# Performance work log

Hardware: AMD Instinct MI355X
Metric: run time of the kernel (lower is better)

## Reference

```python
import jax, jax.numpy as jnp
import numpy as np

B, CIN, COUT, G, HEADS = 4, 256, 256, 8, 4
K, S, P = 7, 1, 3
H = W = 32
IN_W = CIN // G
OUT_W = COUT // G


def setup_inputs() -> dict:
    key = jax.random.key(0)
    ks = jax.random.split(key, 9)
    def n(k, shape, scale=1.0):
        return jax.random.normal(k, shape, dtype=jnp.float32) * scale
    # kaiming fan_out init for the 1x1 convs (fan_out = out channels)
    return {
        "x": n(ks[0], (B, CIN, H, W)),
        "wq": n(ks[1], (G, OUT_W * HEADS, IN_W), (2.0 / (OUT_W * HEADS)) ** 0.5),
        "bq": n(ks[2], (G, OUT_W * HEADS), 0.01),
        "wk": n(ks[3], (G, OUT_W, IN_W), (2.0 / OUT_W) ** 0.5),
        "bk": n(ks[4], (G, OUT_W), 0.01),
        "wv": n(ks[5], (G, OUT_W, IN_W), (2.0 / OUT_W) ** 0.5),
        "bv": n(ks[6], (G, OUT_W), 0.01),
        "rel_h": n(ks[7], (OUT_W // 2, 1, 1, G, K, 1)),
        "rel_w": n(ks[8], (OUT_W // 2, 1, 1, G, 1, K)),
    }


def _sparse_conv(x, w, b):
    # grouped 1x1 conv, groups stacked on last axis (matches torch.stack(dim=-1))
    # x: [B, G*I, h, w]; w: [G, O, I]; b: [G, O] -> [B, O, h, w, G]
    Bn, C, hh, ww = x.shape
    xr = x.reshape(Bn, G, C // G, hh, ww)
    out = jnp.einsum('bgihw,goi->bohwg', xr, w)
    return out + b.T[None, :, None, None, :]


def _unfold(x5, k, s):
    # x5: [B, C, Hp, Wp, G] -> [B, C, Ho, Wo, G, k, k]  (torch unfold(2).unfold(3))
    Bn, C, Hp, Wp, Gn = x5.shape
    Ho = (Hp - k) // s + 1
    Wo = (Wp - k) // s + 1
    patches = jnp.stack(
        [x5[:, :, i:i + (Ho - 1) * s + 1:s, j:j + (Wo - 1) * s + 1:s, :]
         for i in range(k) for j in range(k)], axis=-1)
    return patches.reshape(Bn, C, Ho, Wo, Gn, k, k)


def reference(x, wq, bq, wk, bk, wv, bv, rel_h, rel_w):
    xp = jnp.pad(x, ((0, 0), (0, 0), (P, P), (P, P)))
    q = _sparse_conv(x, wq, bq)    # [B, OUT_W*HEADS, H, W, G]
    k = _sparse_conv(xp, wk, bk)   # [B, OUT_W, Hp, Wp, G] (bias at padded locations, as in torch)
    v = _sparse_conv(xp, wv, bv)
    k = _unfold(k, K, S)           # [B, OUT_W, H, W, G, K, K]
    v = _unfold(v, K, S)
    kh, kw = jnp.split(k, 2, axis=1)
    k = jnp.concatenate([kh + rel_h, kw + rel_w], axis=1)
    kf = k.reshape(B, OUT_W, H, W, G * K * K)
    vf = v.reshape(B, OUT_W, H, W, G * K * K)
    q = q.reshape(B, HEADS, OUT_W, H, W, G)
    # scores: sum over channel c; softmax over flattened (group, kh, kw) window
    scores = jnp.einsum('bhcxyg,bcxym->bhxygm', q, kf)
    attn = jax.nn.softmax(scores, axis=-1)
    # weighted sum over window m and heads h (matches sum(dim=1) then sum(dim=-1))
    out = jnp.einsum('bhxygm,bcxym->bcxyg', attn, vf)   # [B, OUT_W, H, W, G]
    out = jnp.transpose(out, (0, 4, 2, 3, 1)).reshape(B, -1, H, W)  # transpose(1,-1)+reshape
    return out
```

## Files before the change

### kernel.cpp

```cpp
#include <hip/hip_runtime.h>
#include <math.h>

typedef _Float16 f16;
typedef _Float16 f16x4 __attribute__((ext_vector_type(4)));
typedef _Float16 f16x8 __attribute__((ext_vector_type(8)));
typedef __bf16 bf16x4 __attribute__((ext_vector_type(4)));
typedef __bf16 bf16x4a8 __attribute__((ext_vector_type(4), aligned(8)));
typedef short s16x4 __attribute__((ext_vector_type(4)));
typedef float f32x4 __attribute__((ext_vector_type(4)));
typedef unsigned int u32;

#define MFMA_F16(a, b, c)  __builtin_amdgcn_mfma_f32_16x16x32_f16(a, b, c, 0, 0, 0)
#define MFMA_BF16_K16(a, b, c) __builtin_amdgcn_mfma_f32_16x16x16bf16_1k(a, b, c, 0, 0, 0)

static __device__ inline f16x8 cvt8(const float* p) {
    const float4* p4 = (const float4*)p;
    float4 u0 = p4[0], u1 = p4[1];
    f16x8 r;
    r[0] = (f16)u0.x; r[1] = (f16)u0.y; r[2] = (f16)u0.z; r[3] = (f16)u0.w;
    r[4] = (f16)u1.x; r[5] = (f16)u1.y; r[6] = (f16)u1.z; r[7] = (f16)u1.w;
    return r;
}

static __device__ inline u32 alignsel(u32 hi, u32 lo, u32 sh) {
    return sh ? (u32)(((((unsigned long long)hi) << 32) | lo) >> sh) : lo;
}

static __device__ inline u32 pack2bf(float a, float b) {
    __bf16 x0 = (__bf16)a, x1 = (__bf16)b;
    return (u32)__builtin_bit_cast(unsigned short, x0) |
           ((u32)__builtin_bit_cast(unsigned short, x1) << 16);
}

__global__ __launch_bounds__(256) void produce_kernel(
    const float* __restrict__ x,
    const float* __restrict__ wq, const float* __restrict__ bq,
    const float* __restrict__ wk, const float* __restrict__ bk,
    const float* __restrict__ wv, const float* __restrict__ bv,
    const float* __restrict__ rel_h, const float* __restrict__ rel_w,
    f16* __restrict__ Qb, f16* __restrict__ Kb,
    __bf16* __restrict__ Vb, f16* __restrict__ relp) {
    int bid = blockIdx.x;
    int t = threadIdx.x;

    if (bid == 1216) {
        for (int idx = t; idx < 2944; idx += 256) {
            float v;
            if (idx < 896) {
                int c = idx & 15, gk = idx >> 4;
                v = rel_h[c * 56 + gk];
            } else {
                int i2 = idx - 896;
                int c = i2 & 31, gw = i2 >> 5;
                int g = gw >> 3, kw = gw & 7;
                v = (c >= 16 && kw < 7) ? rel_w[(c - 16) * 56 + g * 7 + kw] : 0.f;
            }
            relp[idx] = (f16)v;
        }
        return;
    }

    int hp = bid % 38, g = (bid / 38) & 7, b = bid / 304;
    bool hin = (hp >= 3 && hp < 35);
    size_t kvbase = (size_t)(b * 8 + g);
    u32* Vb32 = (u32*)Vb;

    if (!hin) {
        for (int idx = t; idx < 38 * 32; idx += 256) {
            int wp = idx >> 5, c = idx & 31;
            Kb[((kvbase * 38 + hp) * 38 + wp) * 32 + c] = (f16)bk[g * 32 + c];
        }
        for (int idx = t; idx < 704; idx += 256) {
            int c = idx / 22, dw = idx - c * 22;
            float bb = bv[g * 32 + c];
            float v0 = (dw * 2 <= 37) ? bb : 0.f;
            float v1 = (dw * 2 + 1 <= 37) ? bb : 0.f;
            Vb32[((kvbase * 38 + hp) * 32 + c) * 22 + dw] = pack2bf(v0, v1);
        }
        return;
    }

    int h = hp - 3;
    __shared__ __align__(16) f16 xTl[32 * 40];
    __shared__ float vt[32 * 44];

    {
        int ic = t >> 3, w = (t & 7) * 4;
        float4 xv = *(const float4*)(x + (((size_t)b * 256 + g * 32 + ic) * 32 + h) * 32 + w);
        xTl[(w + 0) * 40 + ic] = (f16)xv.x;
        xTl[(w + 1) * 40 + ic] = (f16)xv.y;
        xTl[(w + 2) * 40 + ic] = (f16)xv.z;
        xTl[(w + 3) * 40 + ic] = (f16)xv.w;
    }
    for (int idx = t; idx < 384; idx += 256) {
        int c = idx & 31, wi = idx >> 5;
        float bb = bv[g * 32 + c];
        if (wi < 3) vt[c * 44 + wi] = bb;
        else if (wi < 6) vt[c * 44 + 32 + wi] = bb;
        else vt[c * 44 + 32 + wi] = 0.f;
    }
    __syncthreads();

    int l15 = t & 15, quad = (t >> 4) & 3, wave = t >> 6;

    f16x8 xf0 = *(const f16x8*)(xTl + l15 * 40 + quad * 8);
    f16x8 xf1 = *(const f16x8*)(xTl + (16 + l15) * 40 + quad * 8);

#pragma unroll
    for (int i = 0; i < 2; ++i) {
        int mq = wave * 2 + i;
        f16x8 wf = cvt8(wq + ((size_t)g * 128 + mq * 16 + l15) * 32 + quad * 8);
        float4 b4 = *(const float4*)(bq + g * 128 + mq * 16 + quad * 4);
#pragma unroll
        for (int Nt = 0; Nt < 2; ++Nt) {
            f32x4 d = {0.f, 0.f, 0.f, 0.f};
            d = MFMA_F16(wf, Nt ? xf1 : xf0, d);
            f16x4 q4;
            q4[0] = (f16)(d[0] + b4.x); q4[1] = (f16)(d[1] + b4.y);
            q4[2] = (f16)(d[2] + b4.z); q4[3] = (f16)(d[3] + b4.w);
            int w = Nt * 16 + l15;
            *(f16x4*)(Qb + (size_t)((b * 32 + h) * 32 + w) * 1024 + g * 128 + mq * 16 + quad * 4) = q4;
        }
    }

    if (wave < 2) {
        f16x8 wf = cvt8(wk + ((size_t)g * 32 + wave * 16 + l15) * 32 + quad * 8);
        float4 b4 = *(const float4*)(bk + g * 32 + wave * 16 + quad * 4);
#pragma unroll
        for (int Nt = 0; Nt < 2; ++Nt) {
            f32x4 d = {0.f, 0.f, 0.f, 0.f};
            d = MFMA_F16(wf, Nt ? xf1 : xf0, d);
            f16x4 k4;
            k4[0] = (f16)(d[0] + b4.x); k4[1] = (f16)(d[1] + b4.y);
            k4[2] = (f16)(d[2] + b4.z); k4[3] = (f16)(d[3] + b4.w);
            int wp = Nt * 16 + l15 + 3;
            *(f16x4*)(Kb + ((kvbase * 38 + hp) * 38 + wp) * 32 + wave * 16 + quad * 4) = k4;
        }
    } else {
        int Nt = wave - 2;
        f16x8 wf = cvt8(wv + ((size_t)g * 32 + Nt * 16 + l15) * 32 + quad * 8);
        float bias = bv[g * 32 + Nt * 16 + l15];
        int c = Nt * 16 + l15;
#pragma unroll
        for (int Mt = 0; Mt < 2; ++Mt) {
            f32x4 d = {0.f, 0.f, 0.f, 0.f};
            d = MFMA_F16(Mt ? xf1 : xf0, wf, d);
            int wp0 = Mt * 16 + quad * 4 + 3;
            vt[c * 44 + wp0 + 0] = d[0] + bias;
            vt[c * 44 + wp0 + 1] = d[1] + bias;
            vt[c * 44 + wp0 + 2] = d[2] + bias;
            vt[c * 44 + wp0 + 3] = d[3] + bias;
        }
    }

    for (int idx = t; idx < 192; idx += 256) {
        int wi = idx >> 5, c = idx & 31;
        int wp = (wi < 3) ? wi : (32 + wi);
        Kb[((kvbase * 38 + hp) * 38 + wp) * 32 + c] = (f16)bk[g * 32 + c];
    }
    __syncthreads();

    for (int idx = t; idx < 704; idx += 256) {
        int c = idx / 22, dw = idx - c * 22;
        Vb32[((kvbase * 38 + hp) * 32 + c) * 22 + dw] =
            pack2bf(vt[c * 44 + dw * 2], vt[c * 44 + dw * 2 + 1]);
    }
}

__global__ __launch_bounds__(512, 1) void attn_kernel(
    const f16* __restrict__ Qb, const f16* __restrict__ Kb,
    const __bf16* __restrict__ Vb, const f16* __restrict__ relp,
    float* __restrict__ out) {
    __shared__ __align__(16) f16 Klds[33600];
    __shared__ __align__(16) __bf16 Vlds[35840];
    __shared__ __align__(16) f16 Trw_l[2048];

    int bid = blockIdx.x;
    int t = threadIdx.x;
    int G = (bid & 7) * 64 + (bid >> 3);
    int yq = G & 3, x = (G >> 2) & 31, b = G >> 7;
    int y0 = yq * 8;
    int b8 = b * 8;

    int wvi = t >> 6;
    int lane = t & 63;
    int l15 = lane & 15, quad = lane >> 4, kwl = lane & 7, p8 = (lane >> 3) & 1;
    bool oddq = (quad & 1);
    int y = y0 + wvi;
    int pid = (b * 32 + x) * 32 + y;

    f16x8 qf[2];
    {
        const f16* qp = Qb + (size_t)pid * 1024;
        qf[0] = *(const f16x8*)(qp + l15 * 32 + quad * 8);
        qf[1] = *(const f16x8*)(qp + (16 + l15) * 32 + quad * 8);
    }

    for (int i = t; i < 3360; i += 512) {
        int row = i >> 2, q = i & 3;
        int g = row / 105, r2 = row - g * 105;
        int kh = r2 / 15, wpl = r2 - kh * 15;
        int wp = y0 + wpl; if (wp > 37) wp = 37;
        f16x8 kv = *(const f16x8*)(Kb + (((size_t)(b8 + g) * 38 + x + kh) * 38 + wp) * 32 + q * 8);
        if (q < 2) kv += *(const f16x8*)(relp + (g * 7 + kh) * 16 + q * 8);
        *(f16x8*)(Klds + row * 40 + q * 8) = kv;
    }
    for (int i = t; i < 8960; i += 512) {
        int row = i / 5, j = i - row * 5;
        int g = row / 224, r2 = row - g * 224;
        int kh = r2 >> 5, c = r2 & 31;
        uint2 v = *(const uint2*)(Vb + (((size_t)(b8 + g) * 38 + x + kh) * 32 + c) * 44 + y0 + j * 4);
        *(uint2*)(Vlds + row * 20 + j * 4) = v;
    }
    {
        int i = t;
        *(uint2*)(Trw_l + i * 4) = *(const uint2*)(relp + 896 + i * 4);
    }
    __syncthreads();

    float fsumT[2] = {0.f, 0.f};
    f32x4 acc[2][2];
#pragma unroll
    for (int ct = 0; ct < 2; ++ct)
#pragma unroll
        for (int m = 0; m < 2; ++m) acc[ct][m] = (f32x4){0.f, 0.f, 0.f, 0.f};

    int wpl37 = 37 - y0;
    int wplk = wvi + kwl; if (wplk > wpl37) wplk = wpl37;
    u32 shsel = (wvi & 1) ? 16u : 0u;
    bool hi4 = (wvi & 2) != 0;
    int eA = ((quad & 1) + (wvi >> 2)) * 4;

#pragma unroll
    for (int chunk = 0; chunk < 4; ++chunk) {
        int gpr = chunk * 2 + p8;
        int gpv = chunk * 2 + (quad >> 1);
        f16x8 rp = *(const f16x8*)(Trw_l + (gpr * 8 + kwl) * 32 + quad * 8);
        const f16* kp = Klds + (gpr * 105 + wplk) * 40 + quad * 8;
        const __bf16* vb0 = Vlds + (size_t)gpv * 4480 + l15 * 20 + eA;
        const __bf16* vb1 = vb0 + 320;
#pragma unroll
        for (int kh = 0; kh < 7; ++kh) {
            f16x8 kb = *(const f16x8*)kp;  kp += 600;
            kb += rp;
            uint2 A0 = *(const uint2*)vb0;
            uint2 B0 = *(const uint2*)(vb0 + 4);
            uint2 A1 = *(const uint2*)vb1;
            uint2 B1 = *(const uint2*)(vb1 + 4);
            vb0 += 640; vb1 += 640;
            u32 a0 = hi4 ? A0.y : A0.x, a1 = hi4 ? B0.x : A0.y, a2 = hi4 ? B0.y : B0.x;
            s16x4 vf0 = __builtin_bit_cast(s16x4,
                make_uint2(alignsel(a1, a0, shsel), alignsel(a2, a1, shsel)));
            u32 c0 = hi4 ? A1.y : A1.x, c1 = hi4 ? B1.x : A1.y, c2 = hi4 ? B1.y : B1.x;
            s16x4 vf1 = __builtin_bit_cast(s16x4,
                make_uint2(alignsel(c1, c0, shsel), alignsel(c2, c1, shsel)));
#pragma unroll
            for (int Mt = 0; Mt < 2; ++Mt) {
                f32x4 d = {0.f, 0.f, 0.f, 0.f};
                d = MFMA_F16(kb, qf[Mt], d);
                float e0 = __expf(d[0]);
                float e1 = __expf(d[1]);
                float e2 = __expf(d[2]);
                float e3 = oddq ? 0.f : __expf(d[3]);
                fsumT[Mt] += (e0 + e1) + (e2 + e3);
                bf16x4 pb;
                pb[0] = (__bf16)e0; pb[1] = (__bf16)e1;
                pb[2] = (__bf16)e2; pb[3] = (__bf16)e3;
                s16x4 pbi = __builtin_bit_cast(s16x4, pb);
                acc[0][Mt] = MFMA_BF16_K16(vf0, pbi, acc[0][Mt]);
                acc[1][Mt] = MFMA_BF16_K16(vf1, pbi, acc[1][Mt]);
            }
        }
    }

#pragma unroll
    for (int m = 0; m < 2; ++m) {
        fsumT[m] += __shfl_xor(fsumT[m], 16);
        fsumT[m] += __shfl_xor(fsumT[m], 32);
    }
    float inv[2] = {1.0f / fsumT[0], 1.0f / fsumT[1]};

#pragma unroll
    for (int Mt = 0; Mt < 2; ++Mt)
#pragma unroll
        for (int ct = 0; ct < 2; ++ct) {
            float v[4];
#pragma unroll
            for (int r = 0; r < 4; ++r) {
                v[r] = acc[ct][Mt][r] * inv[Mt];
                v[r] += __shfl_xor(v[r], 1);
                v[r] += __shfl_xor(v[r], 2);
            }
            if ((l15 & 3) == 0) {
                int g = Mt * 4 + (l15 >> 2);
                float4 o4 = {v[0], v[1], v[2], v[3]};
                *(float4*)(out + ((((size_t)(b8 + g) * 32 + x) * 32 + y) << 5) +
                           ct * 16 + quad * 4) = o4;
            }
        }
}

extern "C" void kernel_launch(void* const* d_in, const int* in_sizes, int n_in,
                              void* d_out, int out_size, void* d_ws, size_t ws_size,
                              hipStream_t stream) {
    const float* x     = (const float*)d_in[0];
    const float* wq    = (const float*)d_in[1];
    const float* bq    = (const float*)d_in[2];
    const float* wk    = (const float*)d_in[3];
    const float* bk    = (const float*)d_in[4];
    const float* wv    = (const float*)d_in[5];
    const float* bv    = (const float*)d_in[6];
    const float* rel_h = (const float*)d_in[7];
    const float* rel_w = (const float*)d_in[8];
    float* out = (float*)d_out;

    unsigned char* ws = (unsigned char*)d_ws;
    f16*    Qb   = (f16*)ws;
    f16*    Kb   = (f16*)(ws + 8388608);
    __bf16* Vb   = (__bf16*)(ws + 8388608 + 2957312);
    f16*    relp = (f16*)(ws + 8388608 + 2957312 + 3424256);

    hipLaunchKernelGGL(produce_kernel, dim3(1217), dim3(256), 0, stream,
                       x, wq, bq, wk, bk, wv, bv, rel_h, rel_w, Qb, Kb, Vb, relp);
    hipLaunchKernelGGL(attn_kernel, dim3(512), dim3(512), 0, stream,
                       Qb, Kb, Vb, relp, out);
}
```

Before: 121.6 us.

## Fuse QKV projection into attention kernel, computing K/V tiles in LDS

Removes the separate produce kernel and its global Q/K/V workspace. Each attention block now loads its 7-row x halo directly from the fp32 input and runs the 1x1 grouped convs with MFMA, writing K (with rel_h folded in), V and Q straight into LDS. This drops one launch and the global round trip of intermediates. In exchange, neighbouring blocks recompute overlapping K/V halo rows, and the x loads are scalar strided reads.

```diff
diff --git a/kernel.cpp b/kernel.cpp
--- a/kernel.cpp
+++ b/kernel.cpp
@@ -5,7 +5,6 @@
 typedef _Float16 f16x4 __attribute__((ext_vector_type(4)));
 typedef _Float16 f16x8 __attribute__((ext_vector_type(8)));
 typedef __bf16 bf16x4 __attribute__((ext_vector_type(4)));
-typedef __bf16 bf16x4a8 __attribute__((ext_vector_type(4), aligned(8)));
 typedef short s16x4 __attribute__((ext_vector_type(4)));
 typedef float f32x4 __attribute__((ext_vector_type(4)));
 typedef unsigned int u32;
@@ -26,159 +25,22 @@
     return sh ? (u32)(((((unsigned long long)hi) << 32) | lo) >> sh) : lo;
 }
 
-static __device__ inline u32 pack2bf(float a, float b) {
-    __bf16 x0 = (__bf16)a, x1 = (__bf16)b;
-    return (u32)__builtin_bit_cast(unsigned short, x0) |
-           ((u32)__builtin_bit_cast(unsigned short, x1) << 16);
-}
-
-__global__ __launch_bounds__(256) void produce_kernel(
+__global__ __launch_bounds__(512, 1) void fused_kernel(
     const float* __restrict__ x,
     const float* __restrict__ wq, const float* __restrict__ bq,
     const float* __restrict__ wk, const float* __restrict__ bk,
     const float* __restrict__ wv, const float* __restrict__ bv,
     const float* __restrict__ rel_h, const float* __restrict__ rel_w,
-    f16* __restrict__ Qb, f16* __restrict__ Kb,
-    __bf16* __restrict__ Vb, f16* __restrict__ relp) {
-    int bid = blockIdx.x;
-    int t = threadIdx.x;
-
-    if (bid == 1216) {
-        for (int idx = t; idx < 2944; idx += 256) {
-            float v;
-            if (idx < 896) {
-                int c = idx & 15, gk = idx >> 4;
-                v = rel_h[c * 56 + gk];
-            } else {
-                int i2 = idx - 896;
-                int c = i2 & 31, gw = i2 >> 5;
-                int g = gw >> 3, kw = gw & 7;
-                v = (c >= 16 && kw < 7) ? rel_w[(c - 16) * 56 + g * 7 + kw] : 0.f;
-            }
-            relp[idx] = (f16)v;
-        }
-        return;
-    }
-
-    int hp = bid % 38, g = (bid / 38) & 7, b = bid / 304;
-    bool hin = (hp >= 3 && hp < 35);
-    size_t kvbase = (size_t)(b * 8 + g);
-    u32* Vb32 = (u32*)Vb;
-
-    if (!hin) {
-        for (int idx = t; idx < 38 * 32; idx += 256) {
-            int wp = idx >> 5, c = idx & 31;
-            Kb[((kvbase * 38 + hp) * 38 + wp) * 32 + c] = (f16)bk[g * 32 + c];
-        }
-        for (int idx = t; idx < 704; idx += 256) {
-            int c = idx / 22, dw = idx - c * 22;
-            float bb = bv[g * 32 + c];
-            float v0 = (dw * 2 <= 37) ? bb : 0.f;
-            float v1 = (dw * 2 + 1 <= 37) ? bb : 0.f;
-            Vb32[((kvbase * 38 + hp) * 32 + c) * 22 + dw] = pack2bf(v0, v1);
-        }
-        return;
-    }
-
-    int h = hp - 3;
-    __shared__ __align__(16) f16 xTl[32 * 40];
-    __shared__ float vt[32 * 44];
-
-    {
-        int ic = t >> 3, w = (t & 7) * 4;
-        float4 xv = *(const float4*)(x + (((size_t)b * 256 + g * 32 + ic) * 32 + h) * 32 + w);
-        xTl[(w + 0) * 40 + ic] = (f16)xv.x;
-        xTl[(w + 1) * 40 + ic] = (f16)xv.y;
-        xTl[(w + 2) * 40 + ic] = (f16)xv.z;
-        xTl[(w + 3) * 40 + ic] = (f16)xv.w;
-    }
-    for (int idx = t; idx < 384; idx += 256) {
-        int c = idx & 31, wi = idx >> 5;
-        float bb = bv[g * 32 + c];
-        if (wi < 3) vt[c * 44 + wi] = bb;
-        else if (wi < 6) vt[c * 44 + 32 + wi] = bb;
-        else vt[c * 44 + 32 + wi] = 0.f;
-    }
-    __syncthreads();
-
-    int l15 = t & 15, quad = (t >> 4) & 3, wave = t >> 6;
-
-    f16x8 xf0 = *(const f16x8*)(xTl + l15 * 40 + quad * 8);
-    f16x8 xf1 = *(const f16x8*)(xTl + (16 + l15) * 40 + quad * 8);
-
-#pragma unroll
-    for (int i = 0; i < 2; ++i) {
-        int mq = wave * 2 + i;
-        f16x8 wf = cvt8(wq + ((size_t)g * 128 + mq * 16 + l15) * 32 + quad * 8);
-        float4 b4 = *(const float4*)(bq + g * 128 + mq * 16 + quad * 4);
-#pragma unroll
-        for (int Nt = 0; Nt < 2; ++Nt) {
-            f32x4 d = {0.f, 0.f, 0.f, 0.f};
-            d = MFMA_F16(wf, Nt ? xf1 : xf0, d);
-            f16x4 q4;
-            q4[0] = (f16)(d[0] + b4.x); q4[1] = (f16)(d[1] + b4.y);
-            q4[2] = (f16)(d[2] + b4.z); q4[3] = (f16)(d[3] + b4.w);
-            int w = Nt * 16 + l15;
-            *(f16x4*)(Qb + (size_t)((b * 32 + h) * 32 + w) * 1024 + g * 128 + mq * 16 + quad * 4) = q4;
-        }
-    }
-
-    if (wave < 2) {
-        f16x8 wf = cvt8(wk + ((size_t)g * 32 + wave * 16 + l15) * 32 + quad * 8);
-        float4 b4 = *(const float4*)(bk + g * 32 + wave * 16 + quad * 4);
-#pragma unroll
-        for (int Nt = 0; Nt < 2; ++Nt) {
-            f32x4 d = {0.f, 0.f, 0.f, 0.f};
-            d = MFMA_F16(wf, Nt ? xf1 : xf0, d);
-            f16x4 k4;
-            k4[0] = (f16)(d[0] + b4.x); k4[1] = (f16)(d[1] + b4.y);
-            k4[2] = (f16)(d[2] + b4.z); k4[3] = (f16)(d[3] + b4.w);
-            int wp = Nt * 16 + l15 + 3;
-            *(f16x4*)(Kb + ((kvbase * 38 + hp) * 38 + wp) * 32 + wave * 16 + quad * 4) = k4;
-        }
-    } else {
-        int Nt = wave - 2;
-        f16x8 wf = cvt8(wv + ((size_t)g * 32 + Nt * 16 + l15) * 32 + quad * 8);
-        float bias = bv[g * 32 + Nt * 16 + l15];
-        int c = Nt * 16 + l15;
-#pragma unroll
-        for (int Mt = 0; Mt < 2; ++Mt) {
-            f32x4 d = {0.f, 0.f, 0.f, 0.f};
-            d = MFMA_F16(Mt ? xf1 : xf0, wf, d);
-            int wp0 = Mt * 16 + quad * 4 + 3;
-            vt[c * 44 + wp0 + 0] = d[0] + bias;
-            vt[c * 44 + wp0 + 1] = d[1] + bias;
-            vt[c * 44 + wp0 + 2] = d[2] + bias;
-            vt[c * 44 + wp0 + 3] = d[3] + bias;
-        }
-    }
-
-    for (int idx = t; idx < 192; idx += 256) {
-        int wi = idx >> 5, c = idx & 31;
-        int wp = (wi < 3) ? wi : (32 + wi);
-        Kb[((kvbase * 38 + hp) * 38 + wp) * 32 + c] = (f16)bk[g * 32 + c];
-    }
-    __syncthreads();
-
-    for (int idx = t; idx < 704; idx += 256) {
-        int c = idx / 22, dw = idx - c * 22;
-        Vb32[((kvbase * 38 + hp) * 32 + c) * 22 + dw] =
-            pack2bf(vt[c * 44 + dw * 2], vt[c * 44 + dw * 2 + 1]);
-    }
-}
-
-__global__ __launch_bounds__(512, 1) void attn_kernel(
-    const f16* __restrict__ Qb, const f16* __restrict__ Kb,
-    const __bf16* __restrict__ Vb, const f16* __restrict__ relp,
     float* __restrict__ out) {
     __shared__ __align__(16) f16 Klds[33600];
     __shared__ __align__(16) __bf16 Vlds[35840];
-    __shared__ __align__(16) f16 Trw_l[2048];
+    __shared__ __align__(16) f16 Qlds[8192];
+    __shared__ __align__(16) f16 TrwL[2048];
 
     int bid = blockIdx.x;
     int t = threadIdx.x;
     int G = (bid & 7) * 64 + (bid >> 3);
-    int yq = G & 3, x = (G >> 2) & 31, b = G >> 7;
+    int yq = G & 3, xx = (G >> 2) & 31, b = G >> 7;
     int y0 = yq * 8;
     int b8 = b * 8;
 
@@ -186,38 +48,90 @@
     int lane = t & 63;
     int l15 = lane & 15, quad = lane >> 4, kwl = lane & 7, p8 = (lane >> 3) & 1;
     bool oddq = (quad & 1);
-    int y = y0 + wvi;
-    int pid = (b * 32 + x) * 32 + y;
-
-    f16x8 qf[2];
+
     {
-        const f16* qp = Qb + (size_t)pid * 1024;
-        qf[0] = *(const f16x8*)(qp + l15 * 32 + quad * 8);
-        qf[1] = *(const f16x8*)(qp + (16 + l15) * 32 + quad * 8);
-    }
-
-    for (int i = t; i < 3360; i += 512) {
-        int row = i >> 2, q = i & 3;
-        int g = row / 105, r2 = row - g * 105;
-        int kh = r2 / 15, wpl = r2 - kh * 15;
-        int wp = y0 + wpl; if (wp > 37) wp = 37;
-        f16x8 kv = *(const f16x8*)(Kb + (((size_t)(b8 + g) * 38 + x + kh) * 38 + wp) * 32 + q * 8);
-        if (q < 2) kv += *(const f16x8*)(relp + (g * 7 + kh) * 16 + q * 8);
-        *(f16x8*)(Klds + row * 40 + q * 8) = kv;
-    }
-    for (int i = t; i < 8960; i += 512) {
-        int row = i / 5, j = i - row * 5;
-        int g = row / 224, r2 = row - g * 224;
-        int kh = r2 >> 5, c = r2 & 31;
-        uint2 v = *(const uint2*)(Vb + (((size_t)(b8 + g) * 38 + x + kh) * 32 + c) * 44 + y0 + j * 4);
-        *(uint2*)(Vlds + row * 20 + j * 4) = v;
-    }
-    {
-        int i = t;
-        *(uint2*)(Trw_l + i * 4) = *(const uint2*)(relp + 896 + i * 4);
+        int g = wvi;
+
+        const float* xb = x + ((size_t)(b * 256 + g * 32 + quad * 8) * 32) * 32;
+        int cX = y0 - 3 + l15;
+        bool cok = ((unsigned)cX < 32u);
+        f16x8 xf[7];
+#pragma unroll
+        for (int rr = 0; rr < 7; ++rr) {
+            int rX = xx - 3 + rr;
+            bool ok = cok && ((unsigned)rX < 32u);
+            int off = rX * 32 + cX;
+#pragma unroll
+            for (int j = 0; j < 8; ++j) {
+                float v = ok ? xb[off + j * 1024] : 0.f;
+                xf[rr][j] = (f16)v;
+            }
+        }
+
+        for (int i = t; i < 2048; i += 512) {
+            int c = i & 31, gw = i >> 5;
+            int g2 = gw >> 3, kw = gw & 7;
+            TrwL[i] = (f16)((c >= 16 && kw < 7) ? rel_w[(c - 16) * 56 + g2 * 7 + kw] : 0.f);
+        }
+
+        f16x8 wkf[2], wvf[2];
+        float4 bk4[2], bv4[2];
+#pragma unroll
+        for (int ct = 0; ct < 2; ++ct) {
+            wkf[ct] = cvt8(wk + ((size_t)g * 32 + ct * 16 + l15) * 32 + quad * 8);
+            wvf[ct] = cvt8(wv + ((size_t)g * 32 + ct * 16 + l15) * 32 + quad * 8);
+            bk4[ct] = *(const float4*)(bk + g * 32 + ct * 16 + quad * 4);
+            bv4[ct] = *(const float4*)(bv + g * 32 + ct * 16 + quad * 4);
+        }
+
+#pragma unroll
+        for (int rr = 0; rr < 7; ++rr) {
+            float rh0 = rel_h[(quad * 4 + 0) * 56 + g * 7 + rr];
+            float rh1 = rel_h[(quad * 4 + 1) * 56 + g * 7 + rr];
+            float rh2 = rel_h[(quad * 4 + 2) * 56 + g * 7 + rr];
+            float rh3 = rel_h[(quad * 4 + 3) * 56 + g * 7 + rr];
+#pragma unroll
+            for (int ct = 0; ct < 2; ++ct) {
+                f32x4 z = {0.f, 0.f, 0.f, 0.f};
+                f32x4 dK = MFMA_F16(wkf[ct], xf[rr], z);
+                f32x4 dV = MFMA_F16(wvf[ct], xf[rr], z);
+                f16x4 k4;
+                k4[0] = (f16)(dK[0] + bk4[ct].x + (ct ? 0.f : rh0));
+                k4[1] = (f16)(dK[1] + bk4[ct].y + (ct ? 0.f : rh1));
+                k4[2] = (f16)(dK[2] + bk4[ct].z + (ct ? 0.f : rh2));
+                k4[3] = (f16)(dK[3] + bk4[ct].w + (ct ? 0.f : rh3));
+                if (l15 < 15)
+                    *(f16x4*)(Klds + ((g * 7 + rr) * 15 + l15) * 40 + ct * 16 + quad * 4) = k4;
+                int vrow = (g * 7 + rr) * 32 + ct * 16 + quad * 4;
+                Vlds[(vrow + 0) * 20 + l15] = (__bf16)(dV[0] + bv4[ct].x);
+                Vlds[(vrow + 1) * 20 + l15] = (__bf16)(dV[1] + bv4[ct].y);
+                Vlds[(vrow + 2) * 20 + l15] = (__bf16)(dV[2] + bv4[ct].z);
+                Vlds[(vrow + 3) * 20 + l15] = (__bf16)(dV[3] + bv4[ct].w);
+            }
+        }
+
+#pragma unroll
+        for (int mq = 0; mq < 8; ++mq) {
+            f16x8 wqf = cvt8(wq + ((size_t)g * 128 + mq * 16 + l15) * 32 + quad * 8);
+            float4 bq4 = *(const float4*)(bq + g * 128 + mq * 16 + quad * 4);
+            f32x4 z = {0.f, 0.f, 0.f, 0.f};
+            f32x4 d = MFMA_F16(wqf, xf[3], z);
+            if (l15 >= 3 && l15 <= 10) {
+                f16x4 q4;
+                q4[0] = (f16)(d[0] + bq4.x); q4[1] = (f16)(d[1] + bq4.y);
+                q4[2] = (f16)(d[2] + bq4.z); q4[3] = (f16)(d[3] + bq4.w);
+                *(f16x4*)(Qlds + (l15 - 3) * 1024 + g * 128 + mq * 16 + quad * 4) = q4;
+            }
+        }
     }
     __syncthreads();
 
+    int y = y0 + wvi;
+
+    f16x8 qf[2];
+    qf[0] = *(const f16x8*)(Qlds + wvi * 1024 + l15 * 32 + quad * 8);
+    qf[1] = *(const f16x8*)(Qlds + wvi * 1024 + 512 + l15 * 32 + quad * 8);
+
     float fsumT[2] = {0.f, 0.f};
     f32x4 acc[2][2];
 #pragma unroll
@@ -225,8 +139,7 @@
 #pragma unroll
         for (int m = 0; m < 2; ++m) acc[ct][m] = (f32x4){0.f, 0.f, 0.f, 0.f};
 
-    int wpl37 = 37 - y0;
-    int wplk = wvi + kwl; if (wplk > wpl37) wplk = wpl37;
+    int wplk = wvi + kwl;
     u32 shsel = (wvi & 1) ? 16u : 0u;
     bool hi4 = (wvi & 2) != 0;
     int eA = ((quad & 1) + (wvi >> 2)) * 4;
@@ -235,7 +148,7 @@
     for (int chunk = 0; chunk < 4; ++chunk) {
         int gpr = chunk * 2 + p8;
         int gpv = chunk * 2 + (quad >> 1);
-        f16x8 rp = *(const f16x8*)(Trw_l + (gpr * 8 + kwl) * 32 + quad * 8);
+        f16x8 rp = *(const f16x8*)(TrwL + (gpr * 8 + kwl) * 32 + quad * 8);
         const f16* kp = Klds + (gpr * 105 + wplk) * 40 + quad * 8;
         const __bf16* vb0 = Vlds + (size_t)gpv * 4480 + l15 * 20 + eA;
         const __bf16* vb1 = vb0 + 320;
@@ -294,7 +207,7 @@
             if ((l15 & 3) == 0) {
                 int g = Mt * 4 + (l15 >> 2);
                 float4 o4 = {v[0], v[1], v[2], v[3]};
-                *(float4*)(out + ((((size_t)(b8 + g) * 32 + x) * 32 + y) << 5) +
+                *(float4*)(out + ((((size_t)(b8 + g) * 32 + xx) * 32 + y) << 5) +
                            ct * 16 + quad * 4) = o4;
             }
         }
@@ -313,15 +226,8 @@
     const float* rel_h = (const float*)d_in[7];
     const float* rel_w = (const float*)d_in[8];
     float* out = (float*)d_out;
-
-    unsigned char* ws = (unsigned char*)d_ws;
-    f16*    Qb   = (f16*)ws;
-    f16*    Kb   = (f16*)(ws + 8388608);
-    __bf16* Vb   = (__bf16*)(ws + 8388608 + 2957312);
-    f16*    relp = (f16*)(ws + 8388608 + 2957312 + 3424256);
-
-    hipLaunchKernelGGL(produce_kernel, dim3(1217), dim3(256), 0, stream,
-                       x, wq, bq, wk, bk, wv, bv, rel_h, rel_w, Qb, Kb, Vb, relp);
-    hipLaunchKernelGGL(attn_kernel, dim3(512), dim3(512), 0, stream,
-                       Qb, Kb, Vb, relp, out);
-}
+    (void)d_ws; (void)ws_size;
+
+    hipLaunchKernelGGL(fused_kernel, dim3(512), dim3(512), 0, stream,
+                       x, wq, bq, wk, bk, wv, bv, rel_h, rel_w, out);
+}
```

Result: slower. 131.1 us (+7.8%).
